# Optimization experiments

Measured on AMD Instinct MI355X. Metric: run time of the kernel, lower is better.

Reference implementation:

```python
import jax, jax.numpy as jnp
import numpy as np

DIM = 4096
N_HEADS = 32
N_KV_HEADS = 8
HEAD_DIM = DIM // N_HEADS
N_REP = N_HEADS // N_KV_HEADS
SEQ_LEN = 2048
ROPE_THETA = 10000.0


def rope_cos_sin(head_dim, seq_len, theta):
    freqs = 1.0 / (theta ** (jnp.arange(0, head_dim, 2, dtype=jnp.float32) / head_dim))  # [hd/2]
    t = jnp.arange(seq_len, dtype=jnp.float32)
    angles = jnp.outer(t, freqs)  # [S, hd/2]
    return jnp.cos(angles), jnp.sin(angles)


def apply_rope(x, cos, sin):
    # x: [B, S, H, hd]; complex rotation on interleaved (even, odd) pairs
    xr = x[..., 0::2].astype(jnp.float32)
    xi = x[..., 1::2].astype(jnp.float32)
    c = cos[None, :, None, :]
    s = sin[None, :, None, :]
    out_r = xr * c - xi * s
    out_i = xr * s + xi * c
    out = jnp.stack([out_r, out_i], axis=-1).reshape(x.shape)
    return out.astype(x.dtype)


def setup_inputs() -> dict:
    key = jax.random.key(0)
    ks = jax.random.split(key, 5)
    x = jax.random.normal(ks[0], (1, SEQ_LEN, DIM), dtype=jnp.float32)
    wq = jax.random.normal(ks[1], (DIM, DIM), dtype=jnp.float32) * (DIM ** -0.5)
    wk = jax.random.normal(ks[2], (N_KV_HEADS * HEAD_DIM, DIM), dtype=jnp.float32) * (DIM ** -0.5)
    wv = jax.random.normal(ks[3], (N_KV_HEADS * HEAD_DIM, DIM), dtype=jnp.float32) * (DIM ** -0.5)
    wo = jax.random.normal(ks[4], (DIM, DIM), dtype=jnp.float32) * (DIM ** -0.5)
    return {"x": x, "start_pos": 0, "wq": wq, "wk": wk, "wv": wv, "wo": wo}


def reference(x, start_pos, wq, wk, wv, wo):
    bsz, seq_len, _ = x.shape
    # projections (torch Linear: y = x @ W.T)
    xq = (x @ wq.T).reshape(bsz, seq_len, N_HEADS, HEAD_DIM)
    xk = (x @ wk.T).reshape(bsz, seq_len, N_KV_HEADS, HEAD_DIM)
    xv = (x @ wv.T).reshape(bsz, seq_len, N_KV_HEADS, HEAD_DIM)

    cos, sin = rope_cos_sin(HEAD_DIM, seq_len, ROPE_THETA)
    xq = apply_rope(xq, cos, sin)
    xk = apply_rope(xk, cos, sin)

    # repeat_kv (GQA): [B, S, Hkv, hd] -> [B, S, Hkv*n_rep, hd]
    keys = jnp.repeat(xk, N_REP, axis=2)
    values = jnp.repeat(xv, N_REP, axis=2)

    # [B, H, S, hd]
    q = xq.transpose(0, 2, 1, 3)
    k = keys.transpose(0, 2, 1, 3)
    v = values.transpose(0, 2, 1, 3)

    scale = 1.0 / jnp.sqrt(jnp.asarray(HEAD_DIM, dtype=jnp.float32))
    scores = jnp.einsum('bhqd,bhkd->bhqk', q, k) * scale  # [B, H, S, S]
    causal = jnp.tril(jnp.ones((seq_len, seq_len), dtype=bool))
    scores = jnp.where(causal[None, None], scores, -jnp.inf)
    attn = jax.nn.softmax(scores.astype(jnp.float32), axis=-1).astype(q.dtype)
    out = jnp.einsum('bhqk,bhkd->bhqd', attn, v)  # [B, H, S, hd]
    out = out.transpose(0, 2, 1, 3).reshape(bsz, seq_len, -1)
    return out @ wo.T
```

## Files before the change

kernel.cpp:

```cpp
#include <hip/hip_runtime.h>

#define DIM 4096
#define KVDIM 1024
#define KVSTRIDE 2048
#define SEQ 2048
#define HEADS 32
#define HD 128

typedef __attribute__((ext_vector_type(8))) short bf16x8;
typedef __attribute__((ext_vector_type(4))) float f32x4;
typedef __attribute__((ext_vector_type(16))) float f32x16;
typedef __attribute__((ext_vector_type(4))) int int4v;

__device__ inline unsigned short f2bf(float f) {
    union { float f; unsigned int u; } v; v.f = f;
    unsigned int r = v.u + 0x7fffu + ((v.u >> 16) & 1u);
    return (unsigned short)(r >> 16);
}
__device__ inline float bf2f(unsigned short h) {
    union { unsigned int u; float f; } v; v.u = ((unsigned int)h) << 16;
    return v.f;
}

__device__ inline void gld16(const void* g, void* l) {
    __builtin_amdgcn_global_load_lds(
        (const __attribute__((address_space(1))) void*)g,
        (__attribute__((address_space(3))) void*)l, 16, 0, 0);
}

__device__ inline unsigned cvtpk(float a, float b) {
    unsigned r;
    asm("v_cvt_pk_bf16_f32 %0, %1, %2" : "=v"(r) : "v"(a), "v"(b));
    return r;
}

__global__ void convert_f32_bf16(const float* __restrict__ in,
                                 unsigned short* __restrict__ out, int n) {
    int i = (blockIdx.x * blockDim.x + threadIdx.x) * 8;
    if (i >= n) return;
    const float4* p = (const float4*)(in + i);
    float4 a = p[0], b = p[1];
    bf16x8 o;
    o[0] = (short)f2bf(a.x); o[1] = (short)f2bf(a.y);
    o[2] = (short)f2bf(a.z); o[3] = (short)f2bf(a.w);
    o[4] = (short)f2bf(b.x); o[5] = (short)f2bf(b.y);
    o[6] = (short)f2bf(b.z); o[7] = (short)f2bf(b.w);
    *(bf16x8*)(out + i) = o;
}

__global__ void rope_table(float* __restrict__ cs, float* __restrict__ sn) {
    int i = blockIdx.x * blockDim.x + threadIdx.x;
    if (i >= SEQ * 64) return;
    int m = i >> 6, f = i & 63;
    float freq = expf(-(float)f * (9.210340371976184f / 64.0f));
    float ang = (float)m * freq;
    float s, c;
    sincosf(ang, &s, &c);
    cs[i] = c; sn[i] = s;
}

__global__ void rope_apply(unsigned short* __restrict__ q, int lppr, int stride, float scale,
                           const float* __restrict__ cs, const float* __restrict__ sn) {
    int i = blockIdx.x * blockDim.x + threadIdx.x;
    int m = i >> lppr;
    int p = i & ((1 << lppr) - 1);
    if (m >= SEQ) return;
    int f = p & 63;
    int col = ((p >> 6) << 7) + (f << 1);
    size_t idx = (size_t)m * stride + col;
    unsigned int u = *(const unsigned int*)&q[idx];
    float xr = bf2f((unsigned short)(u & 0xffffu));
    float xi = bf2f((unsigned short)(u >> 16));
    float c = cs[(m << 6) + f], s = sn[(m << 6) + f];
    float orr = (xr * c - xi * s) * scale;
    float oi  = (xr * s + xi * c) * scale;
    unsigned int w = ((unsigned int)f2bf(oi) << 16) | (unsigned int)f2bf(orr);
    *(unsigned int*)&q[idx] = w;
}

template <bool OUT_BF16>
__global__ __launch_bounds__(256)
void gemm_bt(const unsigned short* __restrict__ A,
             const unsigned short* __restrict__ W,
             void* __restrict__ Cout, int M, int N, int K) {
    __shared__ __align__(16) unsigned short As[128 * 64];
    __shared__ __align__(16) unsigned short Ws[128 * 64];

    int nwg = gridDim.x * gridDim.y;
    int wg = blockIdx.y * gridDim.x + blockIdx.x;
    int cpx = nwg >> 3;
    wg = (wg & 7) * cpx + (wg >> 3);
    int bx = wg % gridDim.x, by = wg / gridDim.x;
    int brow = by * 128, bcol = bx * 128;

    int tid = threadIdx.x, lane = tid & 63, wid = tid >> 6;
    int wr = wid >> 1, wc = wid & 1, l15 = lane & 15, lq = lane >> 4;

    f32x4 acc[4][4] = {};

    for (int bk = 0; bk < K; bk += 64) {
        #pragma unroll
        for (int it = 0; it < 4; ++it) {
            int slot = it * 256 + wid * 64 + lane;
            int r = slot >> 3, g = slot & 7;
            gld16(&A[(size_t)(brow + r) * K + bk + ((g ^ (r & 7)) << 3)],
                  &As[(it * 256 + wid * 64) * 8]);
        }
        #pragma unroll
        for (int it = 0; it < 4; ++it) {
            int slot = it * 256 + wid * 64 + lane;
            int r = slot >> 3, g = slot & 7;
            gld16(&W[(size_t)(bcol + r) * K + bk + ((g ^ (r & 7)) << 3)],
                  &Ws[(it * 256 + wid * 64) * 8]);
        }
        __syncthreads();

        #pragma unroll
        for (int kk = 0; kk < 64; kk += 32) {
            int gb = (kk >> 3) + lq;
            bf16x8 af[4], bfr[4];
            #pragma unroll
            for (int m = 0; m < 4; ++m) {
                int r = wr * 64 + m * 16 + l15;
                af[m] = *(const bf16x8*)&As[r * 64 + ((gb ^ (r & 7)) << 3)];
            }
            #pragma unroll
            for (int n = 0; n < 4; ++n) {
                int r = wc * 64 + n * 16 + l15;
                bfr[n] = *(const bf16x8*)&Ws[r * 64 + ((gb ^ (r & 7)) << 3)];
            }
            #pragma unroll
            for (int m = 0; m < 4; ++m)
                #pragma unroll
                for (int n = 0; n < 4; ++n)
                    acc[m][n] = __builtin_amdgcn_mfma_f32_16x16x32_bf16(
                        af[m], bfr[n], acc[m][n], 0, 0, 0);
        }
        __syncthreads();
    }

    #pragma unroll
    for (int m = 0; m < 4; ++m) {
        #pragma unroll
        for (int n = 0; n < 4; ++n) {
            int row0 = brow + wr * 64 + m * 16 + lq * 4;
            int col = bcol + wc * 64 + n * 16 + l15;
            #pragma unroll
            for (int r = 0; r < 4; ++r) {
                if (OUT_BF16)
                    ((unsigned short*)Cout)[(size_t)(row0 + r) * N + col] = f2bf(acc[m][n][r]);
                else
                    ((float*)Cout)[(size_t)(row0 + r) * N + col] = acc[m][n][r];
            }
        }
    }
}

__global__ __launch_bounds__(256)
void attn_kernel(const unsigned short* __restrict__ Q,
                 const unsigned short* __restrict__ KV,
                 unsigned short* __restrict__ O) {
    __shared__ __align__(16) unsigned short ks[64 * 128];
    __shared__ __align__(16) unsigned short vt[128][66];

    int h = blockIdx.x;
    int yy = (gridDim.y - 1) - blockIdx.y;
    int q0 = yy * 128;
    int kvh = h >> 2;
    int tid = threadIdx.x, lane = tid & 63, wid = tid >> 6;
    int l31 = lane & 31, l5 = lane >> 5;
    int qw0 = q0 + wid * 32;

    bf16x8 qf[8];
    #pragma unroll
    for (int k8 = 0; k8 < 8; ++k8)
        qf[k8] = *(const bf16x8*)&Q[(size_t)(qw0 + l31) * DIM + h * HD + k8 * 16 + l5 * 8];

    f32x16 o_acc[4] = {};
    float m_run = -1e30f, l_run = 0.0f;

    int k4 = tid >> 4;
    int d0 = (tid & 15) * 8;

    int ntiles = (q0 + 128) >> 6;
    for (int t = 0; t < ntiles; ++t) {
        int kv0 = t * 64;
        #pragma unroll
        for (int it = 0; it < 4; ++it) {
            int slot = it * 256 + wid * 64 + lane;
            int r = slot >> 4, g = slot & 15;
            gld16(&KV[(size_t)(kv0 + r) * KVSTRIDE + kvh * HD + ((g ^ (r & 7)) << 3)],
                  &ks[(it * 256 + wid * 64) * 8]);
        }
        {
            bf16x8 v0 = *(const bf16x8*)&KV[(size_t)(kv0 + k4 * 4 + 0) * KVSTRIDE + KVDIM + kvh * HD + d0];
            bf16x8 v1 = *(const bf16x8*)&KV[(size_t)(kv0 + k4 * 4 + 1) * KVSTRIDE + KVDIM + kvh * HD + d0];
            bf16x8 v2 = *(const bf16x8*)&KV[(size_t)(kv0 + k4 * 4 + 2) * KVSTRIDE + KVDIM + kvh * HD + d0];
            bf16x8 v3 = *(const bf16x8*)&KV[(size_t)(kv0 + k4 * 4 + 3) * KVSTRIDE + KVDIM + kvh * HD + d0];
            #pragma unroll
            for (int j = 0; j < 8; ++j) {
                unsigned lo = ((unsigned)(unsigned short)v1[j] << 16) | (unsigned)(unsigned short)v0[j];
                unsigned hi = ((unsigned)(unsigned short)v3[j] << 16) | (unsigned)(unsigned short)v2[j];
                *(unsigned*)&vt[d0 + j][k4 * 4]     = lo;
                *(unsigned*)&vt[d0 + j][k4 * 4 + 2] = hi;
            }
        }
        __syncthreads();

        if (kv0 <= qw0 + 31) {
            #pragma unroll
            for (int sub = 0; sub < 2; ++sub) {
                int kvs = kv0 + sub * 32;
                if (kvs > qw0 + 31) continue;
                f32x16 s = {};
                #pragma unroll
                for (int k8 = 0; k8 < 8; ++k8) {
                    int r = sub * 32 + l31;
                    bf16x8 kf = *(const bf16x8*)&ks[r * 128 + (((k8 * 2 + l5) ^ (r & 7)) << 3)];
                    s = __builtin_amdgcn_mfma_f32_32x32x16_bf16(kf, qf[k8], s, 0, 0, 0);
                }
                if (kvs + 31 > qw0) {
                    #pragma unroll
                    for (int r = 0; r < 16; ++r) {
                        int kv = kvs + (r & 3) + ((r >> 2) << 3) + l5 * 4;
                        if (kv > qw0 + l31) s[r] = -1e30f;
                    }
                }
                float mx = s[0];
                #pragma unroll
                for (int r = 1; r < 16; ++r) mx = fmaxf(mx, s[r]);
                mx = fmaxf(mx, __shfl_xor(mx, 32));
                bool need = mx > m_run + 8.0f;
                if (__any((int)need)) {
                    float mn = fmaxf(m_run, mx);
                    float al = exp2f(m_run - mn);
                    m_run = mn;
                    l_run *= al;
                    #pragma unroll
                    for (int r = 0; r < 16; ++r) {
                        int qlr = (r & 3) + ((r >> 2) << 3) + l5 * 4;
                        float alO = __shfl(al, qlr, 32);
                        #pragma unroll
                        for (int t32 = 0; t32 < 4; ++t32) o_acc[t32][r] *= alO;
                    }
                }
                #pragma unroll
                for (int r = 0; r < 16; ++r) {
                    float p = exp2f(s[r] - m_run);
                    l_run += p;
                    s[r] = p;
                }
                bf16x8 pa[2];
                #pragma unroll
                for (int kk1 = 0; kk1 < 2; ++kk1) {
                    unsigned u0 = cvtpk(s[kk1 * 8 + 0], s[kk1 * 8 + 1]);
                    unsigned u1 = cvtpk(s[kk1 * 8 + 2], s[kk1 * 8 + 3]);
                    unsigned u2 = cvtpk(s[kk1 * 8 + 4], s[kk1 * 8 + 5]);
                    unsigned u3 = cvtpk(s[kk1 * 8 + 6], s[kk1 * 8 + 7]);
                    unsigned t0 = (unsigned)__shfl_xor((int)(l5 ? u0 : u2), 32);
                    unsigned t1 = (unsigned)__shfl_xor((int)(l5 ? u1 : u3), 32);
                    int4v w;
                    w.x = (int)(l5 ? t0 : u0);
                    w.y = (int)(l5 ? t1 : u1);
                    w.z = (int)(l5 ? u2 : t0);
                    w.w = (int)(l5 ? u3 : t1);
                    pa[kk1] = __builtin_bit_cast(bf16x8, w);
                }
                #pragma unroll
                for (int t32 = 0; t32 < 4; ++t32) {
                    #pragma unroll
                    for (int kk1 = 0; kk1 < 2; ++kk1) {
                        const unsigned short* vrow =
                            &vt[t32 * 32 + l31][sub * 32 + kk1 * 16 + l5 * 8];
                        int4v w;
                        w.x = *(const int*)&vrow[0];
                        w.y = *(const int*)&vrow[2];
                        w.z = *(const int*)&vrow[4];
                        w.w = *(const int*)&vrow[6];
                        o_acc[t32] = __builtin_amdgcn_mfma_f32_32x32x16_bf16(
                            pa[kk1], __builtin_bit_cast(bf16x8, w), o_acc[t32], 0, 0, 0);
                    }
                }
            }
        }
        __syncthreads();
    }

    float l_tot = l_run + __shfl_xor(l_run, 32);
    float rinv = __builtin_amdgcn_rcpf(l_tot);
    #pragma unroll
    for (int r = 0; r < 16; ++r) {
        int qlr = (r & 3) + ((r >> 2) << 3) + l5 * 4;
        float rl = __shfl(rinv, qlr, 32);
        #pragma unroll
        for (int t32 = 0; t32 < 4; ++t32)
            O[(size_t)(qw0 + qlr) * DIM + h * HD + t32 * 32 + l31] =
                f2bf(o_acc[t32][r] * rl);
    }
}

extern "C" void kernel_launch(void* const* d_in, const int* in_sizes, int n_in,
                              void* d_out, int out_size, void* d_ws, size_t ws_size,
                              hipStream_t stream) {
    const float* x  = (const float*)d_in[0];
    const float* wq = (const float*)d_in[2];
    const float* wk = (const float*)d_in[3];
    const float* wv = (const float*)d_in[4];
    const float* wo = (const float*)d_in[5];
    float* out = (float*)d_out;

    char* ws = (char*)d_ws;
    unsigned short* xb  = (unsigned short*)(ws);
    unsigned short* qb  = (unsigned short*)(ws + 16777216);
    unsigned short* kvb = (unsigned short*)(ws + 33554432);
    unsigned short* ab  = (unsigned short*)(ws + 41943040);
    float* cs = (float*)(ws + 58720256);
    float* sn = cs + SEQ * 64;
    unsigned short* wscratch = (unsigned short*)d_out;
    unsigned short* wob = (unsigned short*)(ws);

    const float SCALE2 = 0.08838834764831845f * 1.4426950408889634f;

    convert_f32_bf16<<<SEQ * DIM / 2048, 256, 0, stream>>>(x, xb, SEQ * DIM);
    rope_table<<<SEQ * 64 / 256, 256, 0, stream>>>(cs, sn);

    convert_f32_bf16<<<DIM * DIM / 2048, 256, 0, stream>>>(wq, wscratch, DIM * DIM);
    gemm_bt<true><<<dim3(DIM / 128, SEQ / 128), 256, 0, stream>>>(xb, wscratch, qb, SEQ, DIM, DIM);

    convert_f32_bf16<<<KVDIM * DIM / 2048, 256, 0, stream>>>(wk, wscratch, KVDIM * DIM);
    convert_f32_bf16<<<KVDIM * DIM / 2048, 256, 0, stream>>>(wv, wscratch + (size_t)KVDIM * DIM, KVDIM * DIM);
    gemm_bt<true><<<dim3(KVSTRIDE / 128, SEQ / 128), 256, 0, stream>>>(xb, wscratch, kvb, SEQ, KVSTRIDE, DIM);

    rope_apply<<<SEQ * (DIM / 2) / 256, 256, 0, stream>>>(qb, 11, DIM, SCALE2, cs, sn);
    rope_apply<<<SEQ * (KVDIM / 2) / 256, 256, 0, stream>>>(kvb, 9, KVSTRIDE, 1.0f, cs, sn);

    attn_kernel<<<dim3(HEADS, SEQ / 128), 256, 0, stream>>>(qb, kvb, ab);

    convert_f32_bf16<<<DIM * DIM / 2048, 256, 0, stream>>>(wo, wob, DIM * DIM);
    gemm_bt<false><<<dim3(DIM / 128, SEQ / 128), 256, 0, stream>>>(ab, wob, out, SEQ, DIM, DIM);
}
```

Before: 397.9 us.

## Double-buffer K/V tiles in attention kernel and raise MFMA wave priority

Double-buffers the K and transposed V shared-memory tiles so the next tile's global loads (async K copies and V register loads) are issued before the current tile's MFMA work. The V transpose store and a single barrier happen afterward. This is meant to hide global-memory latency behind compute and removes one of the two barriers per tile. It also wraps the MFMA sections in s_setprio. The cost is double the LDS use, which may reduce occupancy, plus extra registers for the prefetched V.

```diff
diff --git a/kernel.cpp b/kernel.cpp
--- a/kernel.cpp
+++ b/kernel.cpp
@@ -160,8 +160,8 @@
 void attn_kernel(const unsigned short* __restrict__ Q,
                  const unsigned short* __restrict__ KV,
                  unsigned short* __restrict__ O) {
-    __shared__ __align__(16) unsigned short ks[64 * 128];
-    __shared__ __align__(16) unsigned short vt[128][66];
+    __shared__ __align__(16) unsigned short ks[2][64 * 128];
+    __shared__ __align__(16) unsigned short vt[2][128][66];
 
     int h = blockIdx.x;
     int yy = (gridDim.y - 1) - blockIdx.y;
@@ -182,30 +182,49 @@
     int k4 = tid >> 4;
     int d0 = (tid & 15) * 8;
 
+    const unsigned short* Kbase = KV + kvh * HD;
+    const unsigned short* Vbase = KV + KVDIM + kvh * HD;
+
     int ntiles = (q0 + 128) >> 6;
+    bf16x8 vr[4];
+
+    #pragma unroll
+    for (int it = 0; it < 4; ++it) {
+        int slot = it * 256 + wid * 64 + lane;
+        int r = slot >> 4, g = slot & 15;
+        gld16(&Kbase[(size_t)r * KVSTRIDE + ((g ^ (r & 7)) << 3)],
+              &ks[0][(it * 256 + wid * 64) * 8]);
+    }
+    #pragma unroll
+    for (int j = 0; j < 4; ++j)
+        vr[j] = *(const bf16x8*)&Vbase[(size_t)(k4 * 4 + j) * KVSTRIDE + d0];
+    asm volatile("s_waitcnt vmcnt(0)" ::: "memory");
+    #pragma unroll
+    for (int j = 0; j < 8; ++j) {
+        unsigned lo = ((unsigned)(unsigned short)vr[1][j] << 16) | (unsigned)(unsigned short)vr[0][j];
+        unsigned hi = ((unsigned)(unsigned short)vr[3][j] << 16) | (unsigned)(unsigned short)vr[2][j];
+        *(unsigned*)&vt[0][d0 + j][k4 * 4]     = lo;
+        *(unsigned*)&vt[0][d0 + j][k4 * 4 + 2] = hi;
+    }
+    __syncthreads();
+
     for (int t = 0; t < ntiles; ++t) {
+        int b = t & 1;
         int kv0 = t * 64;
-        #pragma unroll
-        for (int it = 0; it < 4; ++it) {
-            int slot = it * 256 + wid * 64 + lane;
-            int r = slot >> 4, g = slot & 15;
-            gld16(&KV[(size_t)(kv0 + r) * KVSTRIDE + kvh * HD + ((g ^ (r & 7)) << 3)],
-                  &ks[(it * 256 + wid * 64) * 8]);
-        }
-        {
-            bf16x8 v0 = *(const bf16x8*)&KV[(size_t)(kv0 + k4 * 4 + 0) * KVSTRIDE + KVDIM + kvh * HD + d0];
-            bf16x8 v1 = *(const bf16x8*)&KV[(size_t)(kv0 + k4 * 4 + 1) * KVSTRIDE + KVDIM + kvh * HD + d0];
-            bf16x8 v2 = *(const bf16x8*)&KV[(size_t)(kv0 + k4 * 4 + 2) * KVSTRIDE + KVDIM + kvh * HD + d0];
-            bf16x8 v3 = *(const bf16x8*)&KV[(size_t)(kv0 + k4 * 4 + 3) * KVSTRIDE + KVDIM + kvh * HD + d0];
-            #pragma unroll
-            for (int j = 0; j < 8; ++j) {
-                unsigned lo = ((unsigned)(unsigned short)v1[j] << 16) | (unsigned)(unsigned short)v0[j];
-                unsigned hi = ((unsigned)(unsigned short)v3[j] << 16) | (unsigned)(unsigned short)v2[j];
-                *(unsigned*)&vt[d0 + j][k4 * 4]     = lo;
-                *(unsigned*)&vt[d0 + j][k4 * 4 + 2] = hi;
-            }
-        }
-        __syncthreads();
+        bool pre = (t + 1 < ntiles);
+        if (pre) {
+            int kvn = kv0 + 64;
+            #pragma unroll
+            for (int it = 0; it < 4; ++it) {
+                int slot = it * 256 + wid * 64 + lane;
+                int r = slot >> 4, g = slot & 15;
+                gld16(&Kbase[(size_t)(kvn + r) * KVSTRIDE + ((g ^ (r & 7)) << 3)],
+                      &ks[b ^ 1][(it * 256 + wid * 64) * 8]);
+            }
+            #pragma unroll
+            for (int j = 0; j < 4; ++j)
+                vr[j] = *(const bf16x8*)&Vbase[(size_t)(kvn + k4 * 4 + j) * KVSTRIDE + d0];
+        }
 
         if (kv0 <= qw0 + 31) {
             #pragma unroll
@@ -213,12 +232,14 @@
                 int kvs = kv0 + sub * 32;
                 if (kvs > qw0 + 31) continue;
                 f32x16 s = {};
+                __builtin_amdgcn_s_setprio(1);
                 #pragma unroll
                 for (int k8 = 0; k8 < 8; ++k8) {
                     int r = sub * 32 + l31;
-                    bf16x8 kf = *(const bf16x8*)&ks[r * 128 + (((k8 * 2 + l5) ^ (r & 7)) << 3)];
+                    bf16x8 kf = *(const bf16x8*)&ks[b][r * 128 + (((k8 * 2 + l5) ^ (r & 7)) << 3)];
                     s = __builtin_amdgcn_mfma_f32_32x32x16_bf16(kf, qf[k8], s, 0, 0, 0);
                 }
+                __builtin_amdgcn_s_setprio(0);
                 if (kvs + 31 > qw0) {
                     #pragma unroll
                     for (int r = 0; r < 16; ++r) {
@@ -266,12 +287,13 @@
                     w.w = (int)(l5 ? u3 : t1);
                     pa[kk1] = __builtin_bit_cast(bf16x8, w);
                 }
+                __builtin_amdgcn_s_setprio(1);
                 #pragma unroll
                 for (int t32 = 0; t32 < 4; ++t32) {
                     #pragma unroll
                     for (int kk1 = 0; kk1 < 2; ++kk1) {
                         const unsigned short* vrow =
-                            &vt[t32 * 32 + l31][sub * 32 + kk1 * 16 + l5 * 8];
+                            &vt[b][t32 * 32 + l31][sub * 32 + kk1 * 16 + l5 * 8];
                         int4v w;
                         w.x = *(const int*)&vrow[0];
                         w.y = *(const int*)&vrow[2];
@@ -281,6 +303,18 @@
                             pa[kk1], __builtin_bit_cast(bf16x8, w), o_acc[t32], 0, 0, 0);
                     }
                 }
+                __builtin_amdgcn_s_setprio(0);
+            }
+        }
+
+        if (pre) {
+            asm volatile("s_waitcnt vmcnt(0)" ::: "memory");
+            #pragma unroll
+            for (int j = 0; j < 8; ++j) {
+                unsigned lo = ((unsigned)(unsigned short)vr[1][j] << 16) | (unsigned)(unsigned short)vr[0][j];
+                unsigned hi = ((unsigned)(unsigned short)vr[3][j] << 16) | (unsigned)(unsigned short)vr[2][j];
+                *(unsigned*)&vt[b ^ 1][d0 + j][k4 * 4]     = lo;
+                *(unsigned*)&vt[b ^ 1][d0 + j][k4 * 4 + 2] = hi;
             }
         }
         __syncthreads();
```

Result: no change. 401.6 us (+0.9%).

## Add 512-thread 128x256-tile GEMM with split prefetch and XCD remap for Q/O projections

Applied to the files above, without the earlier changes.

Introduces a new GEMM kernel with 8 waves per block and a 128x256 output tile. It double-buffers swizzled LDS tiles and spreads the next tile's global loads across the two k-substeps, raising MFMA priority around compute. Workgroup IDs are remapped so that neighbouring tiles land on the same XCD. It is used for the Q projection and the output projection, aiming for more reuse per block and better overlap of loads with compute. The trade-offs are more LDS per block (96KB), which limits occupancy, and fewer blocks (256) across the CUs.

```diff
diff --git a/kernel.cpp b/kernel.cpp
--- a/kernel.cpp
+++ b/kernel.cpp
@@ -156,6 +156,125 @@
     }
 }
 
+#define GEMM8_KSTEP(BUF, KS)                                                     \
+    do {                                                                         \
+        int gb = (KS) * 4 + lq;                                                  \
+        bf16x8 af[4], bfr[4];                                                    \
+        _Pragma("unroll") for (int m = 0; m < 4; ++m) {                          \
+            int r = wm * 64 + m * 16 + l15;                                      \
+            af[m] = *(const bf16x8*)&As[BUF][r * 64 + ((gb ^ (r & 7)) << 3)];    \
+        }                                                                        \
+        _Pragma("unroll") for (int n = 0; n < 4; ++n) {                          \
+            int r = wn * 64 + n * 16 + l15;                                      \
+            bfr[n] = *(const bf16x8*)&Ws[BUF][r * 64 + ((gb ^ (r & 7)) << 3)];   \
+        }                                                                        \
+        __builtin_amdgcn_s_setprio(1);                                           \
+        _Pragma("unroll") for (int m = 0; m < 4; ++m)                            \
+            _Pragma("unroll") for (int n = 0; n < 4; ++n)                        \
+                acc[m][n] = __builtin_amdgcn_mfma_f32_16x16x32_bf16(             \
+                    af[m], bfr[n], acc[m][n], 0, 0, 0);                          \
+        __builtin_amdgcn_s_setprio(0);                                           \
+    } while (0)
+
+template <bool OUT_BF16>
+__global__ __launch_bounds__(512)
+void gemm8_bt(const unsigned short* __restrict__ A,
+              const unsigned short* __restrict__ W,
+              void* __restrict__ Cout, int M, int N, int K) {
+    __shared__ __align__(16) unsigned short As[2][128 * 64];
+    __shared__ __align__(16) unsigned short Ws[2][256 * 64];
+
+    int nwg = gridDim.x * gridDim.y;
+    int wg = blockIdx.y * gridDim.x + blockIdx.x;
+    int cpx = nwg >> 3;
+    wg = (wg & 7) * cpx + (wg >> 3);
+    int bx = wg % gridDim.x, by = wg / gridDim.x;
+    int brow = by * 128, bcol = bx * 256;
+
+    int tid = threadIdx.x, lane = tid & 63, wid = tid >> 6;
+    int wm = wid >> 2, wn = wid & 3;
+    int l15 = lane & 15, lq = lane >> 4;
+
+    const unsigned short* Ab = A + (size_t)brow * K;
+    const unsigned short* Wb = W + (size_t)bcol * K;
+
+    f32x4 acc[4][4] = {};
+    int NT = K >> 6;
+
+    #pragma unroll
+    for (int it = 0; it < 2; ++it) {
+        int slot = it * 512 + tid;
+        int r = slot >> 3, g = slot & 7;
+        gld16(&Ab[(size_t)r * K + ((g ^ (r & 7)) << 3)],
+              &As[0][(it * 512 + wid * 64) * 8]);
+    }
+    #pragma unroll
+    for (int it = 0; it < 4; ++it) {
+        int slot = it * 512 + tid;
+        int r = slot >> 3, g = slot & 7;
+        gld16(&Wb[(size_t)r * K + ((g ^ (r & 7)) << 3)],
+              &Ws[0][(it * 512 + wid * 64) * 8]);
+    }
+
+    for (int t = 0; t < NT; ++t) {
+        int b = t & 1;
+        int bkn = (t + 1) << 6;
+        bool pre = (t + 1 < NT);
+
+        if (pre) {
+            #pragma unroll
+            for (int it = 0; it < 2; ++it) {
+                int slot = it * 512 + tid;
+                int r = slot >> 3, g = slot & 7;
+                gld16(&Ab[(size_t)r * K + bkn + ((g ^ (r & 7)) << 3)],
+                      &As[b ^ 1][(it * 512 + wid * 64) * 8]);
+            }
+            {
+                int r = tid >> 3, g = tid & 7;
+                gld16(&Wb[(size_t)r * K + bkn + ((g ^ (r & 7)) << 3)],
+                      &Ws[b ^ 1][(wid * 64) * 8]);
+            }
+            asm volatile("s_waitcnt vmcnt(3)" ::: "memory");
+        } else {
+            asm volatile("s_waitcnt vmcnt(0)" ::: "memory");
+        }
+        __builtin_amdgcn_s_barrier();
+        __builtin_amdgcn_sched_barrier(0);
+        GEMM8_KSTEP(b, 0);
+        __builtin_amdgcn_s_barrier();
+        __builtin_amdgcn_sched_barrier(0);
+
+        if (pre) {
+            #pragma unroll
+            for (int it = 1; it < 4; ++it) {
+                int slot = it * 512 + tid;
+                int r = slot >> 3, g = slot & 7;
+                gld16(&Wb[(size_t)r * K + bkn + ((g ^ (r & 7)) << 3)],
+                      &Ws[b ^ 1][(it * 512 + wid * 64) * 8]);
+            }
+        }
+        GEMM8_KSTEP(b, 1);
+        __builtin_amdgcn_s_barrier();
+        __builtin_amdgcn_sched_barrier(0);
+    }
+
+    #pragma unroll
+    for (int m = 0; m < 4; ++m) {
+        #pragma unroll
+        for (int n = 0; n < 4; ++n) {
+            int row0 = brow + wm * 64 + m * 16 + lq * 4;
+            int col = bcol + wn * 64 + n * 16 + l15;
+            #pragma unroll
+            for (int r = 0; r < 4; ++r) {
+                if (OUT_BF16)
+                    ((unsigned short*)Cout)[(size_t)(row0 + r) * N + col] = f2bf(acc[m][n][r]);
+                else
+                    ((float*)Cout)[(size_t)(row0 + r) * N + col] = acc[m][n][r];
+            }
+        }
+    }
+}
+
 __global__ __launch_bounds__(256)
 void attn_kernel(const unsigned short* __restrict__ Q,
                  const unsigned short* __restrict__ KV,
@@ -325,7 +444,7 @@
     rope_table<<<SEQ * 64 / 256, 256, 0, stream>>>(cs, sn);
 
     convert_f32_bf16<<<DIM * DIM / 2048, 256, 0, stream>>>(wq, wscratch, DIM * DIM);
-    gemm_bt<true><<<dim3(DIM / 128, SEQ / 128), 256, 0, stream>>>(xb, wscratch, qb, SEQ, DIM, DIM);
+    gemm8_bt<true><<<dim3(DIM / 256, SEQ / 128), 512, 0, stream>>>(xb, wscratch, qb, SEQ, DIM, DIM);
 
     convert_f32_bf16<<<KVDIM * DIM / 2048, 256, 0, stream>>>(wk, wscratch, KVDIM * DIM);
     convert_f32_bf16<<<KVDIM * DIM / 2048, 256, 0, stream>>>(wv, wscratch + (size_t)KVDIM * DIM, KVDIM * DIM);
@@ -337,5 +456,5 @@
     attn_kernel<<<dim3(HEADS, SEQ / 128), 256, 0, stream>>>(qb, kvb, ab);
 
     convert_f32_bf16<<<DIM * DIM / 2048, 256, 0, stream>>>(wo, wob, DIM * DIM);
-    gemm_bt<false><<<dim3(DIM / 128, SEQ / 128), 256, 0, stream>>>(ab, wob, out, SEQ, DIM, DIM);
-}
+    gemm8_bt<false><<<dim3(DIM / 256, SEQ / 128), 512, 0, stream>>>(ab, wob, out, SEQ, DIM, DIM);
+}
```

Result: slower. 454.9 us (+14.3%).

## Swizzle V-transpose LDS layout and interleave both QK subtiles with setprio

Applied to the files above, without the earlier changes.

Replaces the padded [128][66] V-transpose LDS buffer with an unpadded 128x64 XOR-swizzled layout, so PV operands load as single 16-byte reads instead of four 4-byte reads, and the transpose stores become 8-byte writes. The two 32-row QK^T subtiles are now computed together in one k8 loop, giving independent MFMA chains, and softmax and PV are then done per subtile. s_setprio is raised around MFMA sections to favour matrix issue across waves. This costs more live registers for the second score tile and adds swizzle index arithmetic.

```diff
diff --git a/kernel.cpp b/kernel.cpp
--- a/kernel.cpp
+++ b/kernel.cpp
@@ -11,6 +11,7 @@
 typedef __attribute__((ext_vector_type(4))) float f32x4;
 typedef __attribute__((ext_vector_type(16))) float f32x16;
 typedef __attribute__((ext_vector_type(4))) int int4v;
+typedef __attribute__((ext_vector_type(2))) unsigned int u32x2;
 
 __device__ inline unsigned short f2bf(float f) {
     union { float f; unsigned int u; } v; v.f = f;
@@ -156,12 +157,64 @@
     }
 }
 
+
+__device__ __forceinline__ void softmax_pack(
+    f32x16& s, f32x16* o_acc, float& m_run, float& l_run,
+    int qw0, int kvs, int l31, int l5, bf16x8* pa) {
+    if (kvs + 31 > qw0) {
+        #pragma unroll
+        for (int r = 0; r < 16; ++r) {
+            int kv = kvs + (r & 3) + ((r >> 2) << 3) + l5 * 4;
+            if (kv > qw0 + l31) s[r] = -1e30f;
+        }
+    }
+    float mx = s[0];
+    #pragma unroll
+    for (int r = 1; r < 16; ++r) mx = fmaxf(mx, s[r]);
+    mx = fmaxf(mx, __shfl_xor(mx, 32));
+    bool need = mx > m_run + 8.0f;
+    if (__any((int)need)) {
+        float mn = fmaxf(m_run, mx);
+        float al = exp2f(m_run - mn);
+        m_run = mn;
+        l_run *= al;
+        #pragma unroll
+        for (int r = 0; r < 16; ++r) {
+            int qlr = (r & 3) + ((r >> 2) << 3) + l5 * 4;
+            float alO = __shfl(al, qlr, 32);
+            #pragma unroll
+            for (int t32 = 0; t32 < 4; ++t32) o_acc[t32][r] *= alO;
+        }
+    }
+    #pragma unroll
+    for (int r = 0; r < 16; ++r) {
+        float p = exp2f(s[r] - m_run);
+        l_run += p;
+        s[r] = p;
+    }
+    #pragma unroll
+    for (int kk1 = 0; kk1 < 2; ++kk1) {
+        unsigned u0 = cvtpk(s[kk1 * 8 + 0], s[kk1 * 8 + 1]);
+        unsigned u1 = cvtpk(s[kk1 * 8 + 2], s[kk1 * 8 + 3]);
+        unsigned u2 = cvtpk(s[kk1 * 8 + 4], s[kk1 * 8 + 5]);
+        unsigned u3 = cvtpk(s[kk1 * 8 + 6], s[kk1 * 8 + 7]);
+        unsigned t0 = (unsigned)__shfl_xor((int)(l5 ? u0 : u2), 32);
+        unsigned t1 = (unsigned)__shfl_xor((int)(l5 ? u1 : u3), 32);
+        int4v w;
+        w.x = (int)(l5 ? t0 : u0);
+        w.y = (int)(l5 ? t1 : u1);
+        w.z = (int)(l5 ? u2 : t0);
+        w.w = (int)(l5 ? u3 : t1);
+        pa[kk1] = __builtin_bit_cast(bf16x8, w);
+    }
+}
+
 __global__ __launch_bounds__(256)
 void attn_kernel(const unsigned short* __restrict__ Q,
                  const unsigned short* __restrict__ KV,
                  unsigned short* __restrict__ O) {
     __shared__ __align__(16) unsigned short ks[64 * 128];
-    __shared__ __align__(16) unsigned short vt[128][66];
+    __shared__ __align__(16) unsigned short vt[128 * 64];
 
     int h = blockIdx.x;
     int yy = (gridDim.y - 1) - blockIdx.y;
@@ -181,6 +234,8 @@
 
     int k4 = tid >> 4;
     int d0 = (tid & 15) * 8;
+    int vhalf = (k4 & 1) * 4;
+    int vgran = k4 >> 1;
 
     int ntiles = (q0 + 128) >> 6;
     for (int t = 0; t < ntiles; ++t) {
@@ -199,88 +254,65 @@
             bf16x8 v3 = *(const bf16x8*)&KV[(size_t)(kv0 + k4 * 4 + 3) * KVSTRIDE + KVDIM + kvh * HD + d0];
             #pragma unroll
             for (int j = 0; j < 8; ++j) {
-                unsigned lo = ((unsigned)(unsigned short)v1[j] << 16) | (unsigned)(unsigned short)v0[j];
-                unsigned hi = ((unsigned)(unsigned short)v3[j] << 16) | (unsigned)(unsigned short)v2[j];
-                *(unsigned*)&vt[d0 + j][k4 * 4]     = lo;
-                *(unsigned*)&vt[d0 + j][k4 * 4 + 2] = hi;
+                int row = d0 + j;
+                int g2 = (vgran ^ (((row >> 3) ^ row) & 7)) << 3;
+                u32x2 w;
+                w.x = ((unsigned)(unsigned short)v1[j] << 16) | (unsigned)(unsigned short)v0[j];
+                w.y = ((unsigned)(unsigned short)v3[j] << 16) | (unsigned)(unsigned short)v2[j];
+                *(u32x2*)&vt[row * 64 + g2 + vhalf] = w;
             }
         }
         __syncthreads();
 
         if (kv0 <= qw0 + 31) {
-            #pragma unroll
-            for (int sub = 0; sub < 2; ++sub) {
-                int kvs = kv0 + sub * 32;
-                if (kvs > qw0 + 31) continue;
-                f32x16 s = {};
+            bool act1 = (kv0 + 32 <= qw0 + 31);
+            f32x16 s0 = {}, s1 = {};
+            __builtin_amdgcn_s_setprio(1);
+            #pragma unroll
+            for (int k8 = 0; k8 < 8; ++k8) {
+                int r0 = l31;
+                bf16x8 kf0 = *(const bf16x8*)&ks[r0 * 128 + (((k8 * 2 + l5) ^ (r0 & 7)) << 3)];
+                s0 = __builtin_amdgcn_mfma_f32_32x32x16_bf16(kf0, qf[k8], s0, 0, 0, 0);
+                if (act1) {
+                    int r1 = 32 + l31;
+                    bf16x8 kf1 = *(const bf16x8*)&ks[r1 * 128 + (((k8 * 2 + l5) ^ (r1 & 7)) << 3)];
+                    s1 = __builtin_amdgcn_mfma_f32_32x32x16_bf16(kf1, qf[k8], s1, 0, 0, 0);
+                }
+            }
+            __builtin_amdgcn_s_setprio(0);
+
+            bf16x8 pa0[2], pa1[2];
+            softmax_pack(s0, o_acc, m_run, l_run, qw0, kv0, l31, l5, pa0);
+            __builtin_amdgcn_s_setprio(1);
+            #pragma unroll
+            for (int t32 = 0; t32 < 4; ++t32) {
+                int d = t32 * 32 + l31;
+                int swz = ((d >> 3) ^ d) & 7;
                 #pragma unroll
-                for (int k8 = 0; k8 < 8; ++k8) {
-                    int r = sub * 32 + l31;
-                    bf16x8 kf = *(const bf16x8*)&ks[r * 128 + (((k8 * 2 + l5) ^ (r & 7)) << 3)];
-                    s = __builtin_amdgcn_mfma_f32_32x32x16_bf16(kf, qf[k8], s, 0, 0, 0);
+                for (int kk1 = 0; kk1 < 2; ++kk1) {
+                    int g = kk1 * 2 + l5;
+                    int4v w = *(const int4v*)&vt[d * 64 + ((g ^ swz) << 3)];
+                    o_acc[t32] = __builtin_amdgcn_mfma_f32_32x32x16_bf16(
+                        pa0[kk1], __builtin_bit_cast(bf16x8, w), o_acc[t32], 0, 0, 0);
                 }
-                if (kvs + 31 > qw0) {
+            }
+            __builtin_amdgcn_s_setprio(0);
+            if (act1) {
+                softmax_pack(s1, o_acc, m_run, l_run, qw0, kv0 + 32, l31, l5, pa1);
+                __builtin_amdgcn_s_setprio(1);
+                #pragma unroll
+                for (int t32 = 0; t32 < 4; ++t32) {
+                    int d = t32 * 32 + l31;
+                    int swz = ((d >> 3) ^ d) & 7;
                     #pragma unroll
-                    for (int r = 0; r < 16; ++r) {
-                        int kv = kvs + (r & 3) + ((r >> 2) << 3) + l5 * 4;
-                        if (kv > qw0 + l31) s[r] = -1e30f;
+                    for (int kk1 = 0; kk1 < 2; ++kk1) {
+                        int g = 4 + kk1 * 2 + l5;
+                        int4v w = *(const int4v*)&vt[d * 64 + ((g ^ swz) << 3)];
+                        o_acc[t32] = __builtin_amdgcn_mfma_f32_32x32x16_bf16(
+                            pa1[kk1], __builtin_bit_cast(bf16x8, w), o_acc[t32], 0, 0, 0);
                     }
                 }
-                float mx = s[0];
-                #pragma unroll
-                for (int r = 1; r < 16; ++r) mx = fmaxf(mx, s[r]);
-                mx = fmaxf(mx, __shfl_xor(mx, 32));
-                bool need = mx > m_run + 8.0f;
-                if (__any((int)need)) {
-                    float mn = fmaxf(m_run, mx);
-                    float al = exp2f(m_run - mn);
-                    m_run = mn;
-                    l_run *= al;
-                    #pragma unroll
-                    for (int r = 0; r < 16; ++r) {
-                        int qlr = (r & 3) + ((r >> 2) << 3) + l5 * 4;
-                        float alO = __shfl(al, qlr, 32);
-                        #pragma unroll
-                        for (int t32 = 0; t32 < 4; ++t32) o_acc[t32][r] *= alO;
-                    }
-                }
-                #pragma unroll
-                for (int r = 0; r < 16; ++r) {
-                    float p = exp2f(s[r] - m_run);
-                    l_run += p;
-                    s[r] = p;
-                }
-                bf16x8 pa[2];
-                #pragma unroll
-                for (int kk1 = 0; kk1 < 2; ++kk1) {
-                    unsigned u0 = cvtpk(s[kk1 * 8 + 0], s[kk1 * 8 + 1]);
-                    unsigned u1 = cvtpk(s[kk1 * 8 + 2], s[kk1 * 8 + 3]);
-                    unsigned u2 = cvtpk(s[kk1 * 8 + 4], s[kk1 * 8 + 5]);
-                    unsigned u3 = cvtpk(s[kk1 * 8 + 6], s[kk1 * 8 + 7]);
-                    unsigned t0 = (unsigned)__shfl_xor((int)(l5 ? u0 : u2), 32);
-                    unsigned t1 = (unsigned)__shfl_xor((int)(l5 ? u1 : u3), 32);
-                    int4v w;
-                    w.x = (int)(l5 ? t0 : u0);
-                    w.y = (int)(l5 ? t1 : u1);
-                    w.z = (int)(l5 ? u2 : t0);
-                    w.w = (int)(l5 ? u3 : t1);
-                    pa[kk1] = __builtin_bit_cast(bf16x8, w);
-                }
-                #pragma unroll
-                for (int t32 = 0; t32 < 4; ++t32) {
-                    #pragma unroll
-                    for (int kk1 = 0; kk1 < 2; ++kk1) {
-                        const unsigned short* vrow =
-                            &vt[t32 * 32 + l31][sub * 32 + kk1 * 16 + l5 * 8];
-                        int4v w;
-                        w.x = *(const int*)&vrow[0];
-                        w.y = *(const int*)&vrow[2];
-                        w.z = *(const int*)&vrow[4];
-                        w.w = *(const int*)&vrow[6];
-                        o_acc[t32] = __builtin_amdgcn_mfma_f32_32x32x16_bf16(
-                            pa[kk1], __builtin_bit_cast(bf16x8, w), o_acc[t32], 0, 0, 0);
-                    }
-                }
+                __builtin_amdgcn_s_setprio(0);
             }
         }
         __syncthreads();
```

New measurement: 403.9 us. Within noise of the previous version (+1.5%).
